# Optimization experiments

Measured on AMD Instinct MI355X. Metric: run time of the kernel, lower is better.

The kernel has to match this reference:

```python
import jax, jax.numpy as jnp
import numpy as np

D_MODEL, D_FFN, N_LEVELS, N_HEADS, N_POINTS = 256, 1024, 4, 8, 4
B, LQ = 2, 8192
SHAPES = [(128, 128), (64, 64), (32, 32), (16, 16)]  # (H_l, W_l) per level
D_HEAD = D_MODEL // N_HEADS


def setup_inputs() -> dict:
    key = jax.random.key(0)
    ks = jax.random.split(key, 16)
    S = sum(h * w for h, w in SHAPES)

    def lin_w(k, fin, fout):
        s = 1.0 / np.sqrt(fin)
        return jax.random.uniform(k, (fin, fout), jnp.float32, -s, s)

    inp = {
        "tgt": jax.random.normal(ks[0], (B, LQ, D_MODEL), jnp.float32),
        "query_pos": jax.random.normal(ks[1], (B, LQ, D_MODEL), jnp.float32),
        "reference_points": jax.random.uniform(ks[2], (B, LQ, N_LEVELS, 2), jnp.float32),
        "src": jax.random.normal(ks[3], (B, S, D_MODEL), jnp.float32),
        "spatial_shapes": np.array(SHAPES, dtype=np.int64),
        "level_start_index": np.concatenate([[0], np.cumsum([h * w for h, w in SHAPES])[:-1]]).astype(np.int64),
        "W_value": lin_w(ks[4], D_MODEL, D_MODEL),
        "b_value": jnp.zeros((D_MODEL,), jnp.float32),
        "W_off": lin_w(ks[5], D_MODEL, N_HEADS * N_LEVELS * N_POINTS * 2),
        "b_off": 0.5 * jax.random.normal(ks[6], (N_HEADS * N_LEVELS * N_POINTS * 2,), jnp.float32),
        "W_attn": lin_w(ks[7], D_MODEL, N_HEADS * N_LEVELS * N_POINTS),
        "b_attn": jnp.zeros((N_HEADS * N_LEVELS * N_POINTS,), jnp.float32),
        "W_out": lin_w(ks[8], D_MODEL, D_MODEL),
        "b_out": jnp.zeros((D_MODEL,), jnp.float32),
        "ln1_g": jnp.ones((D_MODEL,), jnp.float32),
        "ln1_b": jnp.zeros((D_MODEL,), jnp.float32),
        "W1": lin_w(ks[9], D_MODEL, D_FFN),
        "b1": jnp.zeros((D_FFN,), jnp.float32),
        "W2": lin_w(ks[10], D_FFN, D_MODEL),
        "b2": jnp.zeros((D_MODEL,), jnp.float32),
        "ln3_g": jnp.ones((D_MODEL,), jnp.float32),
        "ln3_b": jnp.zeros((D_MODEL,), jnp.float32),
    }
    return inp


def _layer_norm(x, g, b, eps=1e-5):
    mu = jnp.mean(x, -1, keepdims=True)
    var = jnp.mean((x - mu) ** 2, -1, keepdims=True)
    return (x - mu) * jax.lax.rsqrt(var + eps) * g + b


def _ms_deform_attn(q, reference_points, src, shapes,
                    W_value, b_value, W_off, b_off, W_attn, b_attn, W_out, b_out):
    Bq, Lq, _ = q.shape
    value = (src @ W_value + b_value).reshape(Bq, -1, N_HEADS, D_HEAD)
    value = jnp.transpose(value, (0, 2, 1, 3))  # [B, H, S, Dh]
    off = (q @ W_off + b_off).reshape(Bq, Lq, N_HEADS, N_LEVELS, N_POINTS, 2)
    attn = jax.nn.softmax((q @ W_attn + b_attn).reshape(Bq, Lq, N_HEADS, N_LEVELS * N_POINTS), axis=-1)
    attn = attn.reshape(Bq, Lq, N_HEADS, N_LEVELS, N_POINTS)
    # offset normalizer is (W_l, H_l) per level
    normalizer = jnp.array([[w, h] for h, w in shapes], jnp.float32)
    loc = reference_points[:, :, None, :, None, :] + off / normalizer[None, None, None, :, None, :]

    out = jnp.zeros((Bq, Lq, N_HEADS, D_HEAD), jnp.float32)
    start = 0
    for l, (Hl, Wl) in enumerate(shapes):
        Nl = Hl * Wl
        v_l = value[:, :, start:start + Nl]  # [B, H, Nl, Dh]
        start += Nl
        loc_l = jnp.transpose(loc[:, :, :, l, :, :], (0, 2, 1, 3, 4))  # [B, H, Lq, P, 2]
        # grid_sample (align_corners=False, zero padding) pixel coords
        x = loc_l[..., 0] * Wl - 0.5
        y = loc_l[..., 1] * Hl - 0.5
        x0, y0 = jnp.floor(x), jnp.floor(y)
        wx, wy = x - x0, y - y0
        acc = jnp.zeros((Bq, N_HEADS, Lq, N_POINTS, D_HEAD), jnp.float32)
        for dx, dy, w in ((0, 0, (1 - wx) * (1 - wy)), (1, 0, wx * (1 - wy)),
                          (0, 1, (1 - wx) * wy), (1, 1, wx * wy)):
            xi, yi = x0 + dx, y0 + dy
            valid = (xi >= 0) & (xi < Wl) & (yi >= 0) & (yi < Hl)
            idx = (jnp.clip(yi, 0, Hl - 1) * Wl + jnp.clip(xi, 0, Wl - 1)).astype(jnp.int32)
            g = jnp.take_along_axis(v_l, idx.reshape(Bq, N_HEADS, -1, 1), axis=2)
            g = g.reshape(Bq, N_HEADS, Lq, N_POINTS, D_HEAD)
            acc = acc + jnp.where(valid[..., None], w[..., None] * g, 0.0)
        a = jnp.transpose(attn[:, :, :, l, :], (0, 2, 1, 3))  # [B, H, Lq, P]
        out = out + jnp.einsum('bhqp,bhqpd->bqhd', a, acc)
    return out.reshape(Bq, Lq, D_MODEL) @ W_out + b_out


def reference(tgt, query_pos, reference_points, src, spatial_shapes, level_start_index,
              W_value, b_value, W_off, b_off, W_attn, b_attn, W_out, b_out,
              ln1_g, ln1_b, W1, b1, W2, b2, ln3_g, ln3_b):
    shapes = [(int(h), int(w)) for h, w in np.asarray(spatial_shapes)]
    q = tgt + query_pos  # with_pos_embed
    tgt2 = _ms_deform_attn(q, reference_points, src, shapes,
                           W_value, b_value, W_off, b_off, W_attn, b_attn, W_out, b_out)
    x = _layer_norm(tgt + tgt2, ln1_g, ln1_b)  # dropout = identity (eval)
    ff = jax.nn.relu(x @ W1 + b1) @ W2 + b2
    return _layer_norm(x + ff, ln3_g, ln3_b)
```

## Files before the change

### kernel.cpp

```cpp
#include <hip/hip_runtime.h>
#include <hip/hip_bf16.h>
#include <math.h>

#define D_MODEL   256
#define D_FFN     1024
#define N_LEVELS  4
#define N_HEADS   8
#define N_POINTS  4
#define BATCH     2
#define LQ        8192
#define S_TOTAL   21760
#define M_Q       (BATCH*LQ)
#define M_V       (BATCH*S_TOTAL)

typedef __attribute__((ext_vector_type(8))) short bf16x8;
typedef __attribute__((ext_vector_type(4))) float floatx4;

__device__ __forceinline__ void gld_lds16(const void* g, void* l) {
    __builtin_amdgcn_global_load_lds(
        (const __attribute__((address_space(1))) void*)g,
        (__attribute__((address_space(3))) void*)l, 16, 0, 0);
}

template<int BM, int BN, int EPI>
__global__ __launch_bounds__(256)
void mfma_gemm(const __hip_bfloat16* __restrict__ A,
               const __hip_bfloat16* __restrict__ Bt,
               const float* __restrict__ bias, const float* __restrict__ bias2,
               const float* __restrict__ resid,
               const float* __restrict__ lng, const float* __restrict__ lnb,
               float* __restrict__ outf, __hip_bfloat16* __restrict__ outb,
               float* __restrict__ outf2,
               int K, int ldOut)
{
    constexpr int NT  = BN / 16;
    constexpr int AF  = BM / 64;
    constexpr int BCH = BN / 64;

    const int tid  = threadIdx.x;
    const int w    = tid >> 6;
    const int lane = tid & 63;
    const int quad = lane >> 4;
    const int l15  = lane & 15;
    const int row0 = blockIdx.x * BM;
    const int nb0  = blockIdx.y * BN;

    __shared__ alignas(16) short As[BM * 32];
    __shared__ alignas(16) short Bs[BN * 32];

    floatx4 acc[AF][NT];
#pragma unroll
    for (int mi = 0; mi < AF; mi++)
#pragma unroll
        for (int ni = 0; ni < NT; ni++) acc[mi][ni] = (floatx4){0.f, 0.f, 0.f, 0.f};

    const size_t K2 = (size_t)K * 2;

    const char* gA[AF]; short* lA[AF];
#pragma unroll
    for (int i = 0; i < AF; i++) {
        int o = (w * AF + i) * 1024 + lane * 16;
        gA[i] = (const char*)A + (size_t)(row0 + (o >> 6)) * K2 + (o & 63);
        lA[i] = &As[(w * AF + i) * 512];
    }
    const char* gB[BCH]; short* lB[BCH];
#pragma unroll
    for (int j = 0; j < BCH; j++) {
        int o = (w * BCH + j) * 1024 + lane * 16;
        gB[j] = (const char*)Bt + (size_t)(nb0 + (o >> 6)) * K2 + (o & 63);
        lB[j] = &Bs[(w * BCH + j) * 512];
    }

    for (int kt = 0; kt < K; kt += 32) {
        const size_t kb = (size_t)kt * 2;
#pragma unroll
        for (int i = 0; i < AF; i++)  gld_lds16(gA[i] + kb, lA[i]);
#pragma unroll
        for (int j = 0; j < BCH; j++) gld_lds16(gB[j] + kb, lB[j]);
        __syncthreads();

        bf16x8 af[AF];
#pragma unroll
        for (int mi = 0; mi < AF; mi++)
            af[mi] = *(const bf16x8*)&As[(w * (AF * 16) + mi * 16 + l15) * 32 + quad * 8];
#pragma unroll
        for (int ni = 0; ni < NT; ni++) {
            bf16x8 bfr = *(const bf16x8*)&Bs[(ni * 16 + l15) * 32 + quad * 8];
#pragma unroll
            for (int mi = 0; mi < AF; mi++)
                acc[mi][ni] = __builtin_amdgcn_mfma_f32_16x16x32_bf16(af[mi], bfr, acc[mi][ni], 0, 0, 0);
        }
        __syncthreads();
    }

    const bool soft = (EPI == 5) && (blockIdx.y == 2);
    const float* bp = soft ? bias2 : bias;
    const int bcol0 = soft ? 0 : nb0;
    float bias_c[NT];
#pragma unroll
    for (int ni = 0; ni < NT; ni++) bias_c[ni] = bp[bcol0 + ni * 16 + l15];

    if (EPI == 4) {
        float gv[NT], bv[NT];
#pragma unroll
        for (int ni = 0; ni < NT; ni++) { gv[ni] = lng[ni * 16 + l15]; bv[ni] = lnb[ni * 16 + l15]; }
#pragma unroll
        for (int mi = 0; mi < AF; mi++)
#pragma unroll
            for (int r = 0; r < 4; r++) {
                int row = row0 + w * (AF * 16) + mi * 16 + quad * 4 + r;
                size_t rb = (size_t)row * 256;
                float s = 0.f, sq = 0.f, vv[NT];
#pragma unroll
                for (int ni = 0; ni < NT; ni++) {
                    float v = acc[mi][ni][r] + bias_c[ni] + resid[rb + ni * 16 + l15];
                    vv[ni] = v; s += v; sq += v * v;
                }
#pragma unroll
                for (int msk = 1; msk <= 8; msk <<= 1) {
                    s += __shfl_xor(s, msk); sq += __shfl_xor(sq, msk);
                }
                float mean = s * (1.f / 256.f);
                float var  = sq * (1.f / 256.f) - mean * mean;
                float rstd = rsqrtf(var + 1e-5f);
#pragma unroll
                for (int ni = 0; ni < NT; ni++) {
                    float o = (vv[ni] - mean) * rstd * gv[ni] + bv[ni];
                    outf[rb + ni * 16 + l15] = o;
                    if (outb) outb[rb + ni * 16 + l15] = __float2bfloat16(o);
                }
            }
        return;
    }

    if (EPI == 5) {
        if (soft) {
#pragma unroll
            for (int mi = 0; mi < AF; mi++)
#pragma unroll
                for (int r = 0; r < 4; r++) {
                    int row = row0 + w * (AF * 16) + mi * 16 + quad * 4 + r;
                    size_t rb = (size_t)row * 128;
#pragma unroll
                    for (int ni = 0; ni < NT; ni++) {
                        float v = acc[mi][ni][r] + bias_c[ni];
                        float m = v;
#pragma unroll
                        for (int msk = 1; msk <= 8; msk <<= 1) m = fmaxf(m, __shfl_xor(m, msk));
                        float e = __expf(v - m);
                        float ssum = e;
#pragma unroll
                        for (int msk = 1; msk <= 8; msk <<= 1) ssum += __shfl_xor(ssum, msk);
                        outf2[rb + ni * 16 + l15] = e / ssum;
                    }
                }
        } else {
#pragma unroll
            for (int mi = 0; mi < AF; mi++)
#pragma unroll
                for (int r = 0; r < 4; r++) {
                    int row = row0 + w * (AF * 16) + mi * 16 + quad * 4 + r;
                    size_t rb = (size_t)row * 256 + nb0;
#pragma unroll
                    for (int ni = 0; ni < NT; ni++)
                        outf[rb + ni * 16 + l15] = acc[mi][ni][r] + bias_c[ni];
                }
        }
        return;
    }

#pragma unroll
    for (int mi = 0; mi < AF; mi++)
#pragma unroll
        for (int r = 0; r < 4; r++) {
            int row = row0 + w * (AF * 16) + mi * 16 + quad * 4 + r;
            size_t rb = (size_t)row * ldOut + nb0;
#pragma unroll
            for (int ni = 0; ni < NT; ni++) {
                float v = acc[mi][ni][r] + bias_c[ni];
                if (EPI == 2) v = fmaxf(v, 0.f);
                if (EPI == 0) outf[rb + ni * 16 + l15] = v;
                else          outb[rb + ni * 16 + l15] = __float2bfloat16(v);
            }
        }
}

__global__ __launch_bounds__(256)
void transpose_cvt(const float* w0, const float* w1, const float* w2,
                   const float* w3, const float* w4, const float* w5,
                   __hip_bfloat16* o0, __hip_bfloat16* o1, __hip_bfloat16* o2,
                   __hip_bfloat16* o3, __hip_bfloat16* o4, __hip_bfloat16* o5)
{
    int t = blockIdx.x;
    const float* src; __hip_bfloat16* dst; int Kd, Nd, tl;
    if      (t < 64)  { src = w0; dst = o0; Kd = 256;  Nd = 256;  tl = t; }
    else if (t < 128) { src = w1; dst = o1; Kd = 256;  Nd = 256;  tl = t - 64; }
    else if (t < 160) { src = w2; dst = o2; Kd = 256;  Nd = 128;  tl = t - 128; }
    else if (t < 224) { src = w3; dst = o3; Kd = 256;  Nd = 256;  tl = t - 160; }
    else if (t < 480) { src = w4; dst = o4; Kd = 256;  Nd = 1024; tl = t - 224; }
    else              { src = w5; dst = o5; Kd = 1024; Nd = 256;  tl = t - 480; }
    int ntn = Nd >> 5;
    int kt = tl / ntn, nt = tl - kt * ntn;
    __shared__ float T[32][33];
    int tx = threadIdx.x & 31, ty = threadIdx.x >> 5;
#pragma unroll
    for (int i = 0; i < 4; i++) {
        int k = kt * 32 + ty + i * 8;
        T[tx][ty + i * 8] = src[(size_t)k * Nd + nt * 32 + tx];
    }
    __syncthreads();
#pragma unroll
    for (int i = 0; i < 4; i++) {
        int n = nt * 32 + ty + i * 8;
        dst[(size_t)n * Kd + kt * 32 + tx] = __float2bfloat16(T[ty + i * 8][tx]);
    }
}

struct alignas(8) bh4 { __hip_bfloat16 a, b, c, d; };
__global__ __launch_bounds__(256)
void cvt4(const float* __restrict__ in, __hip_bfloat16* __restrict__ o, int n4)
{
    int i = blockIdx.x * 256 + threadIdx.x;
    if (i >= n4) return;
    float4 v = ((const float4*)in)[i];
    ((bh4*)o)[i] = { __float2bfloat16(v.x), __float2bfloat16(v.y),
                     __float2bfloat16(v.z), __float2bfloat16(v.w) };
}

__global__ __launch_bounds__(256)
void addcvt4(const float* __restrict__ a, const float* __restrict__ b,
             __hip_bfloat16* __restrict__ o, int n4)
{
    int i = blockIdx.x * 256 + threadIdx.x;
    if (i >= n4) return;
    float4 x = ((const float4*)a)[i];
    float4 y = ((const float4*)b)[i];
    ((bh4*)o)[i] = { __float2bfloat16(x.x + y.x), __float2bfloat16(x.y + y.y),
                     __float2bfloat16(x.z + y.z), __float2bfloat16(x.w + y.w) };
}

#define QB 4
__global__ __launch_bounds__(256)
void sample_kernel(const float* __restrict__ refp, const float* __restrict__ offb,
                   const float* __restrict__ attn,
                   const __hip_bfloat16* __restrict__ value,
                   __hip_bfloat16* __restrict__ tgt2)
{
    __shared__ int2 spk[QB * 8 * 16 * 4];

    const int q0  = blockIdx.x * QB;
    const int tid = threadIdx.x;

#pragma unroll
    for (int it = tid; it < QB * 8 * 16; it += 256) {
        const int ql = it >> 7, h = (it >> 4) & 7, lp = it & 15;
        const int l = lp >> 2, p = lp & 3;
        const int q = q0 + ql, b = q >> 13;
        const int Wl = 128 >> l;
        const int Hl = Wl;
        const int LSTART = (l == 0) ? 0 : (l == 1) ? 16384 : (l == 2) ? 20480 : 21504;

        const float rx = refp[((size_t)q * N_LEVELS + l) * 2 + 0];
        const float ry = refp[((size_t)q * N_LEVELS + l) * 2 + 1];
        const float ox = offb[(size_t)q * 256 + h * 32 + l * 8 + p * 2 + 0];
        const float oy = offb[(size_t)q * 256 + h * 32 + l * 8 + p * 2 + 1];
        const float a  = attn[(size_t)q * 128 + h * 16 + lp];

        const float x = rx * Wl - 0.5f + ox;
        const float y = ry * Hl - 0.5f + oy;
        const float x0f = floorf(x), y0f = floorf(y);
        const float wx = x - x0f, wy = y - y0f;
        const int ix = (int)x0f, iy = (int)y0f;
        const int base = b * S_TOTAL + LSTART;
        const float cw[4] = {(1.f - wx) * (1.f - wy) * a, wx * (1.f - wy) * a,
                             (1.f - wx) * wy * a,         wx * wy * a};
#pragma unroll
        for (int c = 0; c < 4; c++) {
            const int xi = ix + (c & 1), yi = iy + (c >> 1);
            const bool valid = ((unsigned)xi < (unsigned)Wl) && ((unsigned)yi < (unsigned)Hl);
            const float wv = valid ? cw[c] : 0.f;
            const int pix  = valid ? base + yi * Wl + xi : base;
            spk[it * 4 + c] = make_int2(pix, __float_as_int(wv));
        }
    }
    __syncthreads();

    const int ql = tid >> 6, h = (tid >> 3) & 7, d8 = tid & 7;
    const int q = q0 + ql;
    const int c0 = h * 32 + d8 * 4;
    const char* vb = (const char*)value + (size_t)c0 * 2;

    float a0 = 0.f, a1 = 0.f, a2 = 0.f, a3 = 0.f;
    const int sb = ((ql * 8 + h) * 16) * 4;
#pragma unroll
    for (int lp = 0; lp < 16; lp++)
#pragma unroll
        for (int c = 0; c < 4; c++) {
            int2 pk = spk[sb + lp * 4 + c];
            float wv = __int_as_float(pk.y);
            uint2 rv = *(const uint2*)(vb + ((size_t)(unsigned)pk.x << 9));
            a0 += wv * __uint_as_float(rv.x << 16);
            a1 += wv * __uint_as_float(rv.x & 0xffff0000u);
            a2 += wv * __uint_as_float(rv.y << 16);
            a3 += wv * __uint_as_float(rv.y & 0xffff0000u);
        }

    ((bh4*)(tgt2 + (size_t)q * 256 + c0))[0] =
        { __float2bfloat16(a0), __float2bfloat16(a1),
          __float2bfloat16(a2), __float2bfloat16(a3) };
}

extern "C" void kernel_launch(void* const* d_in, const int* in_sizes, int n_in,
                              void* d_out, int out_size, void* d_ws, size_t ws_size,
                              hipStream_t stream) {
    const float* tgt     = (const float*)d_in[0];
    const float* qpos    = (const float*)d_in[1];
    const float* refp    = (const float*)d_in[2];
    const float* src     = (const float*)d_in[3];
    const float* W_value = (const float*)d_in[6];
    const float* b_value = (const float*)d_in[7];
    const float* W_off   = (const float*)d_in[8];
    const float* b_off   = (const float*)d_in[9];
    const float* W_attn  = (const float*)d_in[10];
    const float* b_attn  = (const float*)d_in[11];
    const float* W_out   = (const float*)d_in[12];
    const float* b_out   = (const float*)d_in[13];
    const float* ln1_g   = (const float*)d_in[14];
    const float* ln1_b   = (const float*)d_in[15];
    const float* W1      = (const float*)d_in[16];
    const float* b1      = (const float*)d_in[17];
    const float* W2      = (const float*)d_in[18];
    const float* b2      = (const float*)d_in[19];
    const float* ln3_g   = (const float*)d_in[20];
    const float* ln3_b   = (const float*)d_in[21];
    float* out = (float*)d_out;

    char* p = (char*)d_ws;
    auto nxt = [&](size_t b) { char* r = p; p += (b + 255) & ~(size_t)255; return r; };
    __hip_bfloat16* Wvt    = (__hip_bfloat16*)nxt((size_t)256 * 256 * 2);
    __hip_bfloat16* Woat   = (__hip_bfloat16*)nxt((size_t)384 * 256 * 2);
    __hip_bfloat16* Woutt  = (__hip_bfloat16*)nxt((size_t)256 * 256 * 2);
    __hip_bfloat16* W1t    = (__hip_bfloat16*)nxt((size_t)1024 * 256 * 2);
    __hip_bfloat16* W2t    = (__hip_bfloat16*)nxt((size_t)256 * 1024 * 2);
    __hip_bfloat16* srcb   = (__hip_bfloat16*)nxt((size_t)M_V * 256 * 2);
    __hip_bfloat16* qb     = (__hip_bfloat16*)nxt((size_t)M_Q * 256 * 2);
    __hip_bfloat16* valueb = (__hip_bfloat16*)nxt((size_t)M_V * 256 * 2);
    float*          offb   = (float*)nxt((size_t)M_Q * 256 * 4);
    float*          attnb  = (float*)nxt((size_t)M_Q * 128 * 4);
    __hip_bfloat16* tgt2b  = (__hip_bfloat16*)nxt((size_t)M_Q * 256 * 2);
    float*          x      = (float*)nxt((size_t)M_Q * 256 * 4);
    __hip_bfloat16* xb     = (__hip_bfloat16*)nxt((size_t)M_Q * 256 * 2);
    __hip_bfloat16* hb     = (__hip_bfloat16*)nxt((size_t)M_Q * 1024 * 2);

    dim3 blk(256);

    transpose_cvt<<<dim3(736), blk, 0, stream>>>(W_value, W_off, W_attn, W_out, W1, W2,
                                                 Wvt, Woat, Woat + 256 * 256, Woutt, W1t, W2t);
    cvt4<<<dim3((M_V * 256 / 4 + 255) / 256), blk, 0, stream>>>(src, srcb, M_V * 256 / 4);
    addcvt4<<<dim3((M_Q * 256 / 4 + 255) / 256), blk, 0, stream>>>(tgt, qpos, qb, M_Q * 256 / 4);

    mfma_gemm<128, 128, 1><<<dim3(M_V / 128, 2), blk, 0, stream>>>(
        srcb, Wvt, b_value, nullptr, nullptr, nullptr, nullptr,
        nullptr, valueb, nullptr, 256, 256);

    mfma_gemm<128, 128, 5><<<dim3(M_Q / 128, 3), blk, 0, stream>>>(
        qb, Woat, b_off, b_attn, nullptr, nullptr, nullptr,
        offb, nullptr, attnb, 256, 256);

    sample_kernel<<<dim3(M_Q / QB), blk, 0, stream>>>(refp, offb, attnb, valueb, tgt2b);

    mfma_gemm<64, 256, 4><<<dim3(M_Q / 64, 1), blk, 0, stream>>>(
        tgt2b, Woutt, b_out, nullptr, tgt, ln1_g, ln1_b, x, xb, nullptr, 256, 256);

    mfma_gemm<128, 128, 2><<<dim3(M_Q / 128, 8), blk, 0, stream>>>(
        xb, W1t, b1, nullptr, nullptr, nullptr, nullptr,
        nullptr, hb, nullptr, 256, 1024);

    mfma_gemm<64, 256, 4><<<dim3(M_Q / 64, 1), blk, 0, stream>>>(
        hb, W2t, b2, nullptr, x, ln3_g, ln3_b, out, nullptr, nullptr, 1024, 256);
}
```

Measured before the change: 314.4 us.

## Double-buffer GEMM loads, merge prep and value/query GEMM launches, widen sampler

The GEMM core now double-buffers its LDS tiles: the next K-slice is prefetched while MFMAs run on the current one, which drops one barrier per iteration, and K becomes a compile-time constant. The three prep kernels are merged into one launch, and the value projection and offset/attention projection GEMMs are merged into a single grid. The sampling kernel handles 8 queries per block with 16-byte gathers and a transposed, padded LDS table. The intent is to hide load latency and cut launch and tail overhead, at the cost of doubled LDS per block (lower occupancy) and one idle column of blocks in the merged GEMM grid.

```diff
diff --git a/kernel.cpp b/kernel.cpp
--- a/kernel.cpp
+++ b/kernel.cpp
@@ -12,9 +12,13 @@
 #define S_TOTAL   21760
 #define M_Q       (BATCH*LQ)
 #define M_V       (BATCH*S_TOTAL)
+#define VTILES    (M_V/128)
 
 typedef __attribute__((ext_vector_type(8))) short bf16x8;
 typedef __attribute__((ext_vector_type(4))) float floatx4;
+
+struct alignas(8)  bh4 { __hip_bfloat16 a, b, c, d; };
+struct alignas(16) bh8 { __hip_bfloat16 v[8]; };
 
 __device__ __forceinline__ void gld_lds16(const void* g, void* l) {
     __builtin_amdgcn_global_load_lds(
@@ -22,83 +26,102 @@
         (__attribute__((address_space(3))) void*)l, 16, 0, 0);
 }
 
-template<int BM, int BN, int EPI>
-__global__ __launch_bounds__(256)
-void mfma_gemm(const __hip_bfloat16* __restrict__ A,
-               const __hip_bfloat16* __restrict__ Bt,
-               const float* __restrict__ bias, const float* __restrict__ bias2,
-               const float* __restrict__ resid,
-               const float* __restrict__ lng, const float* __restrict__ lnb,
-               float* __restrict__ outf, __hip_bfloat16* __restrict__ outb,
-               float* __restrict__ outf2,
-               int K, int ldOut)
+template<int BM, int BN, int K>
+__device__ __forceinline__ void gemm_core(const __hip_bfloat16* __restrict__ A,
+                                          const __hip_bfloat16* __restrict__ Bt,
+                                          int row0, int nb0,
+                                          short* As, short* Bs,
+                                          floatx4 (&acc)[BM/64][BN/16])
 {
     constexpr int NT  = BN / 16;
     constexpr int AF  = BM / 64;
     constexpr int BCH = BN / 64;
+    constexpr int NIT = K / 32;
 
     const int tid  = threadIdx.x;
     const int w    = tid >> 6;
     const int lane = tid & 63;
     const int quad = lane >> 4;
     const int l15  = lane & 15;
-    const int row0 = blockIdx.x * BM;
-    const int nb0  = blockIdx.y * BN;
-
-    __shared__ alignas(16) short As[BM * 32];
-    __shared__ alignas(16) short Bs[BN * 32];
-
-    floatx4 acc[AF][NT];
-#pragma unroll
-    for (int mi = 0; mi < AF; mi++)
-#pragma unroll
-        for (int ni = 0; ni < NT; ni++) acc[mi][ni] = (floatx4){0.f, 0.f, 0.f, 0.f};
-
     const size_t K2 = (size_t)K * 2;
 
-    const char* gA[AF]; short* lA[AF];
+    const char* gA[AF]; int lA[AF];
 #pragma unroll
     for (int i = 0; i < AF; i++) {
         int o = (w * AF + i) * 1024 + lane * 16;
         gA[i] = (const char*)A + (size_t)(row0 + (o >> 6)) * K2 + (o & 63);
-        lA[i] = &As[(w * AF + i) * 512];
-    }
-    const char* gB[BCH]; short* lB[BCH];
+        lA[i] = (w * AF + i) * 512;
+    }
+    const char* gB[BCH]; int lB[BCH];
 #pragma unroll
     for (int j = 0; j < BCH; j++) {
         int o = (w * BCH + j) * 1024 + lane * 16;
         gB[j] = (const char*)Bt + (size_t)(nb0 + (o >> 6)) * K2 + (o & 63);
-        lB[j] = &Bs[(w * BCH + j) * 512];
-    }
-
-    for (int kt = 0; kt < K; kt += 32) {
-        const size_t kb = (size_t)kt * 2;
-#pragma unroll
-        for (int i = 0; i < AF; i++)  gld_lds16(gA[i] + kb, lA[i]);
-#pragma unroll
-        for (int j = 0; j < BCH; j++) gld_lds16(gB[j] + kb, lB[j]);
+        lB[j] = (w * BCH + j) * 512;
+    }
+
+#pragma unroll
+    for (int i = 0; i < AF; i++)  gld_lds16(gA[i], &As[lA[i]]);
+#pragma unroll
+    for (int j = 0; j < BCH; j++) gld_lds16(gB[j], &Bs[lB[j]]);
+
+#pragma unroll 8
+    for (int it = 0; it < NIT; ++it) {
         __syncthreads();
-
+        const int cb = it & 1;
+        if (it + 1 < NIT) {
+            const size_t kb = (size_t)(it + 1) * 64;
+            const int nb = cb ^ 1;
+#pragma unroll
+            for (int i = 0; i < AF; i++)  gld_lds16(gA[i] + kb, &As[nb * BM * 32 + lA[i]]);
+#pragma unroll
+            for (int j = 0; j < BCH; j++) gld_lds16(gB[j] + kb, &Bs[nb * BN * 32 + lB[j]]);
+        }
+        const short* Ab = &As[cb * BM * 32];
+        const short* Bb = &Bs[cb * BN * 32];
         bf16x8 af[AF];
 #pragma unroll
         for (int mi = 0; mi < AF; mi++)
-            af[mi] = *(const bf16x8*)&As[(w * (AF * 16) + mi * 16 + l15) * 32 + quad * 8];
+            af[mi] = *(const bf16x8*)&Ab[(w * (AF * 16) + mi * 16 + l15) * 32 + quad * 8];
 #pragma unroll
         for (int ni = 0; ni < NT; ni++) {
-            bf16x8 bfr = *(const bf16x8*)&Bs[(ni * 16 + l15) * 32 + quad * 8];
+            bf16x8 bfr = *(const bf16x8*)&Bb[(ni * 16 + l15) * 32 + quad * 8];
 #pragma unroll
             for (int mi = 0; mi < AF; mi++)
                 acc[mi][ni] = __builtin_amdgcn_mfma_f32_16x16x32_bf16(af[mi], bfr, acc[mi][ni], 0, 0, 0);
         }
-        __syncthreads();
-    }
-
-    const bool soft = (EPI == 5) && (blockIdx.y == 2);
-    const float* bp = soft ? bias2 : bias;
-    const int bcol0 = soft ? 0 : nb0;
+    }
+}
+
+template<int BM, int BN, int K, int EPI>
+__global__ __launch_bounds__(256)
+void mfma_gemm(const __hip_bfloat16* __restrict__ A,
+               const __hip_bfloat16* __restrict__ Bt,
+               const float* __restrict__ bias,
+               const float* __restrict__ resid,
+               const float* __restrict__ lng, const float* __restrict__ lnb,
+               float* __restrict__ outf, __hip_bfloat16* __restrict__ outb,
+               int ldOut)
+{
+    constexpr int NT = BN / 16, AF = BM / 64;
+    __shared__ alignas(16) short As[2 * BM * 32];
+    __shared__ alignas(16) short Bs[2 * BN * 32];
+
+    const int tid = threadIdx.x, w = tid >> 6, lane = tid & 63;
+    const int quad = lane >> 4, l15 = lane & 15;
+    const int row0 = blockIdx.x * BM, nb0 = blockIdx.y * BN;
+
+    floatx4 acc[AF][NT];
+#pragma unroll
+    for (int mi = 0; mi < AF; mi++)
+#pragma unroll
+        for (int ni = 0; ni < NT; ni++) acc[mi][ni] = (floatx4){0.f, 0.f, 0.f, 0.f};
+
+    gemm_core<BM, BN, K>(A, Bt, row0, nb0, As, Bs, acc);
+
     float bias_c[NT];
 #pragma unroll
-    for (int ni = 0; ni < NT; ni++) bias_c[ni] = bp[bcol0 + ni * 16 + l15];
+    for (int ni = 0; ni < NT; ni++) bias_c[ni] = bias[nb0 + ni * 16 + l15];
 
     if (EPI == 4) {
         float gv[NT], bv[NT];
@@ -133,42 +156,6 @@
         return;
     }
 
-    if (EPI == 5) {
-        if (soft) {
-#pragma unroll
-            for (int mi = 0; mi < AF; mi++)
-#pragma unroll
-                for (int r = 0; r < 4; r++) {
-                    int row = row0 + w * (AF * 16) + mi * 16 + quad * 4 + r;
-                    size_t rb = (size_t)row * 128;
-#pragma unroll
-                    for (int ni = 0; ni < NT; ni++) {
-                        float v = acc[mi][ni][r] + bias_c[ni];
-                        float m = v;
-#pragma unroll
-                        for (int msk = 1; msk <= 8; msk <<= 1) m = fmaxf(m, __shfl_xor(m, msk));
-                        float e = __expf(v - m);
-                        float ssum = e;
-#pragma unroll
-                        for (int msk = 1; msk <= 8; msk <<= 1) ssum += __shfl_xor(ssum, msk);
-                        outf2[rb + ni * 16 + l15] = e / ssum;
-                    }
-                }
-        } else {
-#pragma unroll
-            for (int mi = 0; mi < AF; mi++)
-#pragma unroll
-                for (int r = 0; r < 4; r++) {
-                    int row = row0 + w * (AF * 16) + mi * 16 + quad * 4 + r;
-                    size_t rb = (size_t)row * 256 + nb0;
-#pragma unroll
-                    for (int ni = 0; ni < NT; ni++)
-                        outf[rb + ni * 16 + l15] = acc[mi][ni][r] + bias_c[ni];
-                }
-        }
-        return;
-    }
-
 #pragma unroll
     for (int mi = 0; mi < AF; mi++)
 #pragma unroll
@@ -177,88 +164,167 @@
             size_t rb = (size_t)row * ldOut + nb0;
 #pragma unroll
             for (int ni = 0; ni < NT; ni++) {
-                float v = acc[mi][ni][r] + bias_c[ni];
-                if (EPI == 2) v = fmaxf(v, 0.f);
-                if (EPI == 0) outf[rb + ni * 16 + l15] = v;
-                else          outb[rb + ni * 16 + l15] = __float2bfloat16(v);
+                float v = fmaxf(acc[mi][ni][r] + bias_c[ni], 0.f);
+                outb[rb + ni * 16 + l15] = __float2bfloat16(v);
             }
         }
 }
 
 __global__ __launch_bounds__(256)
-void transpose_cvt(const float* w0, const float* w1, const float* w2,
-                   const float* w3, const float* w4, const float* w5,
-                   __hip_bfloat16* o0, __hip_bfloat16* o1, __hip_bfloat16* o2,
-                   __hip_bfloat16* o3, __hip_bfloat16* o4, __hip_bfloat16* o5)
+void mfma_gemm_vq(const __hip_bfloat16* __restrict__ srcb,
+                  const __hip_bfloat16* __restrict__ Wvt,
+                  const float* __restrict__ b_value,
+                  __hip_bfloat16* __restrict__ valueb,
+                  const __hip_bfloat16* __restrict__ qb,
+                  const __hip_bfloat16* __restrict__ Woat,
+                  const float* __restrict__ b_off, const float* __restrict__ b_attn,
+                  float* __restrict__ offb, float* __restrict__ attnb)
 {
-    int t = blockIdx.x;
-    const float* src; __hip_bfloat16* dst; int Kd, Nd, tl;
-    if      (t < 64)  { src = w0; dst = o0; Kd = 256;  Nd = 256;  tl = t; }
-    else if (t < 128) { src = w1; dst = o1; Kd = 256;  Nd = 256;  tl = t - 64; }
-    else if (t < 160) { src = w2; dst = o2; Kd = 256;  Nd = 128;  tl = t - 128; }
-    else if (t < 224) { src = w3; dst = o3; Kd = 256;  Nd = 256;  tl = t - 160; }
-    else if (t < 480) { src = w4; dst = o4; Kd = 256;  Nd = 1024; tl = t - 224; }
-    else              { src = w5; dst = o5; Kd = 1024; Nd = 256;  tl = t - 480; }
-    int ntn = Nd >> 5;
-    int kt = tl / ntn, nt = tl - kt * ntn;
-    __shared__ float T[32][33];
-    int tx = threadIdx.x & 31, ty = threadIdx.x >> 5;
-#pragma unroll
-    for (int i = 0; i < 4; i++) {
-        int k = kt * 32 + ty + i * 8;
-        T[tx][ty + i * 8] = src[(size_t)k * Nd + nt * 32 + tx];
-    }
-    __syncthreads();
-#pragma unroll
-    for (int i = 0; i < 4; i++) {
-        int n = nt * 32 + ty + i * 8;
-        dst[(size_t)n * Kd + kt * 32 + tx] = __float2bfloat16(T[ty + i * 8][tx]);
-    }
-}
-
-struct alignas(8) bh4 { __hip_bfloat16 a, b, c, d; };
+    __shared__ alignas(16) short As[2 * 128 * 32];
+    __shared__ alignas(16) short Bs[2 * 128 * 32];
+
+    const bool isV = blockIdx.x < VTILES;
+    if (isV && blockIdx.y == 2) return;
+
+    const int tid = threadIdx.x, w = tid >> 6, lane = tid & 63;
+    const int quad = lane >> 4, l15 = lane & 15;
+    const int nb0 = blockIdx.y * 128;
+
+    floatx4 acc[2][8];
+#pragma unroll
+    for (int mi = 0; mi < 2; mi++)
+#pragma unroll
+        for (int ni = 0; ni < 8; ni++) acc[mi][ni] = (floatx4){0.f, 0.f, 0.f, 0.f};
+
+    if (isV) {
+        const int row0 = blockIdx.x * 128;
+        gemm_core<128, 128, 256>(srcb, Wvt, row0, nb0, As, Bs, acc);
+        float bias_c[8];
+#pragma unroll
+        for (int ni = 0; ni < 8; ni++) bias_c[ni] = b_value[nb0 + ni * 16 + l15];
+#pragma unroll
+        for (int mi = 0; mi < 2; mi++)
+#pragma unroll
+            for (int r = 0; r < 4; r++) {
+                int row = row0 + w * 32 + mi * 16 + quad * 4 + r;
+                size_t rb = (size_t)row * 256 + nb0;
+#pragma unroll
+                for (int ni = 0; ni < 8; ni++)
+                    valueb[rb + ni * 16 + l15] = __float2bfloat16(acc[mi][ni][r] + bias_c[ni]);
+            }
+        return;
+    }
+
+    const int row0 = (blockIdx.x - VTILES) * 128;
+    gemm_core<128, 128, 256>(qb, Woat, row0, nb0, As, Bs, acc);
+
+    if (blockIdx.y < 2) {
+        float bias_c[8];
+#pragma unroll
+        for (int ni = 0; ni < 8; ni++) bias_c[ni] = b_off[nb0 + ni * 16 + l15];
+#pragma unroll
+        for (int mi = 0; mi < 2; mi++)
+#pragma unroll
+            for (int r = 0; r < 4; r++) {
+                int row = row0 + w * 32 + mi * 16 + quad * 4 + r;
+                size_t rb = (size_t)row * 256 + nb0;
+#pragma unroll
+                for (int ni = 0; ni < 8; ni++)
+                    offb[rb + ni * 16 + l15] = acc[mi][ni][r] + bias_c[ni];
+            }
+    } else {
+        float bias_c[8];
+#pragma unroll
+        for (int ni = 0; ni < 8; ni++) bias_c[ni] = b_attn[ni * 16 + l15];
+#pragma unroll
+        for (int mi = 0; mi < 2; mi++)
+#pragma unroll
+            for (int r = 0; r < 4; r++) {
+                int row = row0 + w * 32 + mi * 16 + quad * 4 + r;
+                size_t rb = (size_t)row * 128;
+#pragma unroll
+                for (int ni = 0; ni < 8; ni++) {
+                    float v = acc[mi][ni][r] + bias_c[ni];
+                    float m = v;
+#pragma unroll
+                    for (int msk = 1; msk <= 8; msk <<= 1) m = fmaxf(m, __shfl_xor(m, msk));
+                    float e = __expf(v - m);
+                    float ssum = e;
+#pragma unroll
+                    for (int msk = 1; msk <= 8; msk <<= 1) ssum += __shfl_xor(ssum, msk);
+                    attnb[rb + ni * 16 + l15] = e / ssum;
+                }
+            }
+    }
+}
+
 __global__ __launch_bounds__(256)
-void cvt4(const float* __restrict__ in, __hip_bfloat16* __restrict__ o, int n4)
+void prep_kernel(const float* w0, const float* w1, const float* w2,
+                 const float* w3, const float* w4, const float* w5,
+                 __hip_bfloat16* o0, __hip_bfloat16* o1, __hip_bfloat16* o2,
+                 __hip_bfloat16* o3, __hip_bfloat16* o4, __hip_bfloat16* o5,
+                 const float* src, __hip_bfloat16* srcb,
+                 const float* tgt, const float* qpos, __hip_bfloat16* qb)
 {
-    int i = blockIdx.x * 256 + threadIdx.x;
-    if (i >= n4) return;
-    float4 v = ((const float4*)in)[i];
-    ((bh4*)o)[i] = { __float2bfloat16(v.x), __float2bfloat16(v.y),
-                     __float2bfloat16(v.z), __float2bfloat16(v.w) };
-}
-
-__global__ __launch_bounds__(256)
-void addcvt4(const float* __restrict__ a, const float* __restrict__ b,
-             __hip_bfloat16* __restrict__ o, int n4)
-{
-    int i = blockIdx.x * 256 + threadIdx.x;
-    if (i >= n4) return;
-    float4 x = ((const float4*)a)[i];
-    float4 y = ((const float4*)b)[i];
-    ((bh4*)o)[i] = { __float2bfloat16(x.x + y.x), __float2bfloat16(x.y + y.y),
-                     __float2bfloat16(x.z + y.z), __float2bfloat16(x.w + y.w) };
-}
-
-#define QB 4
+    const int bx = blockIdx.x;
+    if (bx < 736) {
+        int t = bx;
+        const float* s; __hip_bfloat16* dst; int Kd, Nd, tl;
+        if      (t < 64)  { s = w0; dst = o0; Kd = 256;  Nd = 256;  tl = t; }
+        else if (t < 128) { s = w1; dst = o1; Kd = 256;  Nd = 256;  tl = t - 64; }
+        else if (t < 160) { s = w2; dst = o2; Kd = 256;  Nd = 128;  tl = t - 128; }
+        else if (t < 224) { s = w3; dst = o3; Kd = 256;  Nd = 256;  tl = t - 160; }
+        else if (t < 480) { s = w4; dst = o4; Kd = 256;  Nd = 1024; tl = t - 224; }
+        else              { s = w5; dst = o5; Kd = 1024; Nd = 256;  tl = t - 480; }
+        int ntn = Nd >> 5;
+        int kt = tl / ntn, nt = tl - kt * ntn;
+        __shared__ float T[32][33];
+        int tx = threadIdx.x & 31, ty = threadIdx.x >> 5;
+#pragma unroll
+        for (int i = 0; i < 4; i++) {
+            int k = kt * 32 + ty + i * 8;
+            T[tx][ty + i * 8] = s[(size_t)k * Nd + nt * 32 + tx];
+        }
+        __syncthreads();
+#pragma unroll
+        for (int i = 0; i < 4; i++) {
+            int n = nt * 32 + ty + i * 8;
+            dst[(size_t)n * Kd + kt * 32 + tx] = __float2bfloat16(T[ty + i * 8][tx]);
+        }
+    } else if (bx < 736 + 10880) {
+        int i = (bx - 736) * 256 + threadIdx.x;
+        float4 v = ((const float4*)src)[i];
+        ((bh4*)srcb)[i] = { __float2bfloat16(v.x), __float2bfloat16(v.y),
+                            __float2bfloat16(v.z), __float2bfloat16(v.w) };
+    } else {
+        int i = (bx - 736 - 10880) * 256 + threadIdx.x;
+        float4 x = ((const float4*)tgt)[i];
+        float4 y = ((const float4*)qpos)[i];
+        ((bh4*)qb)[i] = { __float2bfloat16(x.x + y.x), __float2bfloat16(x.y + y.y),
+                          __float2bfloat16(x.z + y.z), __float2bfloat16(x.w + y.w) };
+    }
+}
+
+#define QB 8
 __global__ __launch_bounds__(256)
 void sample_kernel(const float* __restrict__ refp, const float* __restrict__ offb,
                    const float* __restrict__ attn,
                    const __hip_bfloat16* __restrict__ value,
                    __hip_bfloat16* __restrict__ tgt2)
 {
-    __shared__ int2 spk[QB * 8 * 16 * 4];
+    __shared__ int2 spk[64 * 65];
 
     const int q0  = blockIdx.x * QB;
     const int tid = threadIdx.x;
 
 #pragma unroll
-    for (int it = tid; it < QB * 8 * 16; it += 256) {
+    for (int k = 0; k < 4; k++) {
+        const int it = tid + k * 256;
         const int ql = it >> 7, h = (it >> 4) & 7, lp = it & 15;
         const int l = lp >> 2, p = lp & 3;
         const int q = q0 + ql, b = q >> 13;
         const int Wl = 128 >> l;
-        const int Hl = Wl;
-        const int LSTART = (l == 0) ? 0 : (l == 1) ? 16384 : (l == 2) ? 20480 : 21504;
+        const int LST = (l == 0) ? 0 : (l == 1) ? 16384 : (l == 2) ? 20480 : 21504;
 
         const float rx = refp[((size_t)q * N_LEVELS + l) * 2 + 0];
         const float ry = refp[((size_t)q * N_LEVELS + l) * 2 + 1];
@@ -267,47 +333,49 @@
         const float a  = attn[(size_t)q * 128 + h * 16 + lp];
 
         const float x = rx * Wl - 0.5f + ox;
-        const float y = ry * Hl - 0.5f + oy;
+        const float y = ry * Wl - 0.5f + oy;
         const float x0f = floorf(x), y0f = floorf(y);
         const float wx = x - x0f, wy = y - y0f;
         const int ix = (int)x0f, iy = (int)y0f;
-        const int base = b * S_TOTAL + LSTART;
+        const int base = b * S_TOTAL + LST;
+        const int g = ql * 8 + h;
         const float cw[4] = {(1.f - wx) * (1.f - wy) * a, wx * (1.f - wy) * a,
                              (1.f - wx) * wy * a,         wx * wy * a};
 #pragma unroll
         for (int c = 0; c < 4; c++) {
             const int xi = ix + (c & 1), yi = iy + (c >> 1);
-            const bool valid = ((unsigned)xi < (unsigned)Wl) && ((unsigned)yi < (unsigned)Hl);
-            const float wv = valid ? cw[c] : 0.f;
-            const int pix  = valid ? base + yi * Wl + xi : base;
-            spk[it * 4 + c] = make_int2(pix, __float_as_int(wv));
+            const bool valid = ((unsigned)xi < (unsigned)Wl) && ((unsigned)yi < (unsigned)Wl);
+            spk[(lp * 4 + c) * 65 + g] =
+                make_int2(valid ? base + yi * Wl + xi : base,
+                          __float_as_int(valid ? cw[c] : 0.f));
         }
     }
     __syncthreads();
 
-    const int ql = tid >> 6, h = (tid >> 3) & 7, d8 = tid & 7;
-    const int q = q0 + ql;
-    const int c0 = h * 32 + d8 * 4;
+    const int ql = tid >> 5, h = (tid >> 2) & 7, d4 = tid & 3;
+    const int q = q0 + ql, g = ql * 8 + h;
+    const int c0 = h * 32 + d4 * 8;
     const char* vb = (const char*)value + (size_t)c0 * 2;
 
-    float a0 = 0.f, a1 = 0.f, a2 = 0.f, a3 = 0.f;
-    const int sb = ((ql * 8 + h) * 16) * 4;
-#pragma unroll
-    for (int lp = 0; lp < 16; lp++)
-#pragma unroll
-        for (int c = 0; c < 4; c++) {
-            int2 pk = spk[sb + lp * 4 + c];
-            float wv = __int_as_float(pk.y);
-            uint2 rv = *(const uint2*)(vb + ((size_t)(unsigned)pk.x << 9));
-            a0 += wv * __uint_as_float(rv.x << 16);
-            a1 += wv * __uint_as_float(rv.x & 0xffff0000u);
-            a2 += wv * __uint_as_float(rv.y << 16);
-            a3 += wv * __uint_as_float(rv.y & 0xffff0000u);
-        }
-
-    ((bh4*)(tgt2 + (size_t)q * 256 + c0))[0] =
-        { __float2bfloat16(a0), __float2bfloat16(a1),
-          __float2bfloat16(a2), __float2bfloat16(a3) };
+    float ac[8] = {0.f, 0.f, 0.f, 0.f, 0.f, 0.f, 0.f, 0.f};
+#pragma unroll
+    for (int sc = 0; sc < 64; sc++) {
+        int2 pk = spk[sc * 65 + g];
+        float wv = __int_as_float(pk.y);
+        uint4 rv = *(const uint4*)(vb + ((size_t)(unsigned)pk.x << 9));
+        ac[0] += wv * __uint_as_float(rv.x << 16);
+        ac[1] += wv * __uint_as_float(rv.x & 0xffff0000u);
+        ac[2] += wv * __uint_as_float(rv.y << 16);
+        ac[3] += wv * __uint_as_float(rv.y & 0xffff0000u);
+        ac[4] += wv * __uint_as_float(rv.z << 16);
+        ac[5] += wv * __uint_as_float(rv.z & 0xffff0000u);
+        ac[6] += wv * __uint_as_float(rv.w << 16);
+        ac[7] += wv * __uint_as_float(rv.w & 0xffff0000u);
+    }
+    bh8 o;
+#pragma unroll
+    for (int i = 0; i < 8; i++) o.v[i] = __float2bfloat16(ac[i]);
+    *(bh8*)(tgt2 + (size_t)q * 256 + c0) = o;
 }
 
 extern "C" void kernel_launch(void* const* d_in, const int* in_sizes, int n_in,
@@ -354,28 +422,22 @@
 
     dim3 blk(256);
 
-    transpose_cvt<<<dim3(736), blk, 0, stream>>>(W_value, W_off, W_attn, W_out, W1, W2,
-                                                 Wvt, Woat, Woat + 256 * 256, Woutt, W1t, W2t);
-    cvt4<<<dim3((M_V * 256 / 4 + 255) / 256), blk, 0, stream>>>(src, srcb, M_V * 256 / 4);
-    addcvt4<<<dim3((M_Q * 256 / 4 + 255) / 256), blk, 0, stream>>>(tgt, qpos, qb, M_Q * 256 / 4);
-
-    mfma_gemm<128, 128, 1><<<dim3(M_V / 128, 2), blk, 0, stream>>>(
-        srcb, Wvt, b_value, nullptr, nullptr, nullptr, nullptr,
-        nullptr, valueb, nullptr, 256, 256);
-
-    mfma_gemm<128, 128, 5><<<dim3(M_Q / 128, 3), blk, 0, stream>>>(
-        qb, Woat, b_off, b_attn, nullptr, nullptr, nullptr,
-        offb, nullptr, attnb, 256, 256);
+    prep_kernel<<<dim3(736 + 10880 + 4096), blk, 0, stream>>>(
+        W_value, W_off, W_attn, W_out, W1, W2,
+        Wvt, Woat, Woat + 256 * 256, Woutt, W1t, W2t,
+        src, srcb, tgt, qpos, qb);
+
+    mfma_gemm_vq<<<dim3(VTILES + M_Q / 128, 3), blk, 0, stream>>>(
+        srcb, Wvt, b_value, valueb, qb, Woat, b_off, b_attn, offb, attnb);
 
     sample_kernel<<<dim3(M_Q / QB), blk, 0, stream>>>(refp, offb, attnb, valueb, tgt2b);
 
-    mfma_gemm<64, 256, 4><<<dim3(M_Q / 64, 1), blk, 0, stream>>>(
-        tgt2b, Woutt, b_out, nullptr, tgt, ln1_g, ln1_b, x, xb, nullptr, 256, 256);
-
-    mfma_gemm<128, 128, 2><<<dim3(M_Q / 128, 8), blk, 0, stream>>>(
-        xb, W1t, b1, nullptr, nullptr, nullptr, nullptr,
-        nullptr, hb, nullptr, 256, 1024);
-
-    mfma_gemm<64, 256, 4><<<dim3(M_Q / 64, 1), blk, 0, stream>>>(
-        hb, W2t, b2, nullptr, x, ln3_g, ln3_b, out, nullptr, nullptr, 1024, 256);
-}
+    mfma_gemm<64, 256, 256, 4><<<dim3(M_Q / 64, 1), blk, 0, stream>>>(
+        tgt2b, Woutt, b_out, tgt, ln1_g, ln1_b, x, xb, 256);
+
+    mfma_gemm<128, 128, 256, 2><<<dim3(M_Q / 128, 8), blk, 0, stream>>>(
+        xb, W1t, b1, nullptr, nullptr, nullptr, nullptr, hb, 1024);
+
+    mfma_gemm<64, 256, 1024, 4><<<dim3(M_Q / 64, 1), blk, 0, stream>>>(
+        hb, W2t, b2, x, ln3_g, ln3_b, out, nullptr, 256);
+}
```

New measurement: 306.8 us. 1.02x faster.
